# Kernel tuning notes

Hardware: AMD Instinct MI355X
Metric: run time of the kernel (lower is better)

## Reference

```python
import jax, jax.numpy as jnp
import numpy as np

G = 64          # offset groups == weight groups
KH = KW = 3
K = KH * KW
STRIDE = 2
PAD = 1


def _conv2d(x, w, b):
    out = jax.lax.conv_general_dilated(
        x, w, (STRIDE, STRIDE), [(PAD, PAD), (PAD, PAD)],
        dimension_numbers=("NCHW", "OIHW", "NCHW"))
    return out + b[None, :, None, None]


def _deform_core(x, offset, mask, w_deform):
    B, C, H, W = x.shape
    Ho, Wo = offset.shape[2], offset.shape[3]
    Cg = C // G
    # torchvision layout: channel = ((g*K + k)*2 + {0:dy,1:dx})
    off = offset.reshape(B, G, K, 2, Ho, Wo)
    dy, dx = off[:, :, :, 0], off[:, :, :, 1]          # [B,G,K,Ho,Wo]
    ki = (jnp.arange(K) // KW).astype(x.dtype)
    kj = (jnp.arange(K) % KW).astype(x.dtype)
    base_y = (jnp.arange(Ho, dtype=x.dtype) * STRIDE - PAD)[None, :, None] + ki[:, None, None]  # [K,Ho,1]
    base_x = (jnp.arange(Wo, dtype=x.dtype) * STRIDE - PAD)[None, None, :] + kj[:, None, None]  # [K,1,Wo]
    py = dy + base_y[None, None]                        # [B,G,K,Ho,Wo]
    px = dx + base_x[None, None]

    xg = x.reshape(B, G, Cg, H * W)
    y0 = jnp.floor(py)
    x0 = jnp.floor(px)
    wy = py - y0
    wx = px - x0
    KHW = K * Ho * Wo

    def gather(yc, xc, wgt):
        valid = (yc >= 0) & (yc <= H - 1) & (xc >= 0) & (xc <= W - 1)
        idx = (jnp.clip(yc, 0, H - 1) * W + jnp.clip(xc, 0, W - 1)).astype(jnp.int32)
        idx = jnp.broadcast_to(idx.reshape(B, G, 1, KHW), (B, G, Cg, KHW))
        v = jnp.take_along_axis(xg, idx, axis=3)
        return v * (wgt * valid.astype(x.dtype)).reshape(B, G, 1, KHW)

    val = (gather(y0, x0, (1 - wy) * (1 - wx))
           + gather(y0, x0 + 1, (1 - wy) * wx)
           + gather(y0 + 1, x0, wy * (1 - wx))
           + gather(y0 + 1, x0 + 1, wy * wx))
    cols = val.reshape(B, G, Cg, K, Ho, Wo) * mask.reshape(B, G, 1, K, Ho, Wo)
    # grouped conv as einsum: w_deform [C_out, Cg, 3, 3] -> [G, C_out//G, Cg, K]
    wg = w_deform.reshape(G, w_deform.shape[0] // G, Cg, K)
    out = jnp.einsum("bgckhw,gock->bgohw", cols, wg)
    return out.reshape(B, w_deform.shape[0], Ho, Wo)


def setup_inputs() -> dict:
    key = jax.random.key(0)
    ks = jax.random.split(key, 6)
    B, C, H, W = 2, 128, 256, 256
    x = jax.random.normal(ks[0], (B, C, H, W), dtype=jnp.float32)
    # small offset weights so sampled locations stay near the regular grid
    w_offset = jax.random.normal(ks[1], (G * 2 * K, C, 3, 3), dtype=jnp.float32) * 0.01
    b_offset = jax.random.normal(ks[2], (G * 2 * K,), dtype=jnp.float32) * 0.1
    w_mask = jax.random.normal(ks[3], (G * K, C, 3, 3), dtype=jnp.float32) * 0.01
    b_mask = jax.random.normal(ks[4], (G * K,), dtype=jnp.float32) * 0.1
    w_deform = jax.random.normal(ks[5], (C, C // G, 3, 3), dtype=jnp.float32) * (1.0 / np.sqrt((C // G) * K))
    return {"x": x, "w_offset": w_offset, "b_offset": b_offset,
            "w_mask": w_mask, "b_mask": b_mask, "w_deform": w_deform}


def reference(x, w_offset, b_offset, w_mask, b_mask, w_deform):
    offset = _conv2d(x, w_offset, b_offset)
    mask = jax.nn.sigmoid(_conv2d(x, w_mask, b_mask))
    return _deform_core(x, offset, mask, w_deform)
```

## Files before the change

kernel.cpp:

```cpp
#include <hip/hip_runtime.h>
#include <math.h>

#define B_SZ 2
#define H_IN 256
#define W_IN 256
#define HO 128
#define WO 128
#define CIN 128
#define CO_OFF 1152
#define CO_MSK 576
#define NG 64
#define KD 1152
#define KBY 2304
#define ND 32768
#define MPAD 1792
#define NT 18
#define XTROW_B 66048
#define XTIMG_B 17040384

typedef short short8 __attribute__((ext_vector_type(8)));
typedef float f32x4 __attribute__((ext_vector_type(4)));
typedef const unsigned int __attribute__((address_space(1))) gcu32;
typedef unsigned int __attribute__((address_space(3))) slu32;

__device__ __forceinline__ unsigned short f2b(float v) {
  union { float f; unsigned u; } a; a.f = v;
  unsigned r = a.u + 0x7FFF + ((a.u >> 16) & 1);
  return (unsigned short)(r >> 16);
}
__device__ __forceinline__ float b2f(unsigned short u) {
  union { unsigned u; float f; } a; a.u = ((unsigned)u) << 16;
  return a.f;
}

__global__ __launch_bounds__(256) void xpose(const float* __restrict__ x,
                                             unsigned short* __restrict__ xt) {
  const int bid = blockIdx.x;
  const int iyt = bid % 258;
  const int b = bid / 258;
  const int tid = threadIdx.x;
  char* rowp = (char*)xt + (size_t)b * XTIMG_B + (size_t)iyt * XTROW_B;
  const int iy = iyt - 1;
  const short8 z8 = {0, 0, 0, 0, 0, 0, 0, 0};

  if (iy < 0 || iy >= H_IN) {
    for (int i = tid; i < 4128; i += 256)
      *reinterpret_cast<short8*>(rowp + i * 16) = z8;
    return;
  }
  if (tid < 32) {
    int c = tid & 15;
    *reinterpret_cast<short8*>(rowp + ((tid >> 4) ? 257 * 256 : 0) + c * 16) = z8;
  }

  __shared__ float sX[32][68];
  const float* xb = x + (size_t)b * CIN * 65536 + iy * 256;
  for (int ci0 = 0; ci0 < CIN; ci0 += 32) {
    for (int ix0 = 0; ix0 < W_IN; ix0 += 64) {
      __syncthreads();
      {
        int ci_l = tid >> 3, f4 = tid & 7;
        const float4* src = reinterpret_cast<const float4*>(
            xb + (size_t)(ci0 + ci_l) * 65536 + ix0);
        *reinterpret_cast<float4*>(&sX[ci_l][f4 * 4]) = src[f4];
        *reinterpret_cast<float4*>(&sX[ci_l][(f4 + 8) * 4]) = src[f4 + 8];
      }
      __syncthreads();
      {
        int ix_l = tid >> 2, cq = (tid & 3) * 8;
        short8 o;
        #pragma unroll
        for (int e = 0; e < 8; e++) o[e] = (short)f2b(sX[cq + e][ix_l]);
        *reinterpret_cast<short8*>(rowp + (ix0 + ix_l + 1) * 256 + (ci0 + cq) * 2) = o;
      }
    }
  }
}

__global__ __launch_bounds__(256) void pack_w(const float* __restrict__ w_off,
                                              const float* __restrict__ w_msk,
                                              unsigned short* __restrict__ wb) {
  int i = blockIdx.x * 256 + threadIdx.x;
  int m = i / KD;
  int k = i - m * KD;
  int tap = k >> 7, ci = k & 127;
  int src = ci * 9 + tap;
  float v = 0.f;
  if (m < CO_OFF) v = w_off[(size_t)m * KD + src];
  else if (m < 1728) v = w_msk[(size_t)(m - CO_OFF) * KD + src];
  wb[i] = f2b(v);
}

__global__ __launch_bounds__(256, 2) void gemm_conv(
    const unsigned short* __restrict__ wb, const unsigned short* __restrict__ xt,
    const float* __restrict__ b_off, const float* __restrict__ b_msk,
    unsigned short* __restrict__ offs, unsigned short* __restrict__ mask)
{
  __shared__ __attribute__((aligned(128))) char lds[2][32768];

  const int bid = blockIdx.x;
  const int swz = (bid & 7) * 448 + (bid >> 3);
  const int m0 = (swz % 14) * 128;
  const int n0 = (swz / 14) * 128;
  const int ho = (n0 >> 7) & 127;
  const int b  = n0 >> 14;

  const int tid = threadIdx.x;
  const int l = tid & 63;
  const int w = tid >> 6;

  const int rl = l >> 3;
  const int kbsw = ((l & 7) << 4) ^ (rl << 4);

  const char* gA = (const char*)wb + (size_t)(m0 + (w & 1) * 64 + rl) * KBY + kbsw;
  const char* pB = (const char*)xt + (size_t)b * XTIMG_B
                 + ((w & 1) * 64 + rl) * 512 + kbsw;
  const int sb_off = (w & 1) * 8192;

  const int fr = l & 15;
  const int kq = (l >> 4) << 4;
  const int wm = (w >> 1) * 64;
  const int wn = (w & 1) * 64;

  f32x4 acc[4][4];
  #pragma unroll
  for (int a = 0; a < 4; a++)
    #pragma unroll
    for (int c = 0; c < 4; c++) acc[a][c] = (f32x4)(0.f);

  auto STAGE = [&](int kt, int bf) {
    if (w < 2) {
      const char* pa = gA + kt * 128;
      #pragma unroll
      for (int j = 0; j < 8; j++)
        __builtin_amdgcn_global_load_lds((gcu32*)(pa + (size_t)j * 8 * KBY),
                                         (slu32*)(&lds[bf][sb_off + j * 1024]), 16, 0, 0);
    } else {
      int tap = kt >> 1;
      int kh = (tap * 11) >> 5;
      int kw = tap - 3 * kh;
      const char* pb = pB + (2 * ho + kh) * XTROW_B + kw * 256 + (kt & 1) * 128;
      #pragma unroll
      for (int j = 0; j < 8; j++)
        __builtin_amdgcn_global_load_lds((gcu32*)(pb + j * 4096),
                                         (slu32*)(&lds[bf][16384 + sb_off + j * 1024]), 16, 0, 0);
    }
  };

  STAGE(0, 0);
  __syncthreads();

  int cur = 0;
  for (int t = 0; t < NT; t++) {
    if (t < NT - 1) STAGE(t + 1, cur ^ 1);

    const char* bufA = &lds[cur][0];
    const char* bufB = &lds[cur][16384];
    #pragma unroll
    for (int kk = 0; kk < 2; kk++) {
      short8 af[4], bf[4];
      #pragma unroll
      for (int mi = 0; mi < 4; mi++) {
        int row = wm + mi * 16 + fr;
        af[mi] = *(const short8*)(bufA + row * 128 + ((kk * 64 + kq) ^ ((row & 7) << 4)));
      }
      #pragma unroll
      for (int ni = 0; ni < 4; ni++) {
        int row = wn + ni * 16 + fr;
        bf[ni] = *(const short8*)(bufB + row * 128 + ((kk * 64 + kq) ^ ((row & 7) << 4)));
      }
      __builtin_amdgcn_s_setprio(1);
      #pragma unroll
      for (int mi = 0; mi < 4; mi++)
        #pragma unroll
        for (int ni = 0; ni < 4; ni++)
          asm("v_mfma_f32_16x16x32_bf16 %0, %1, %2, %0"
              : "+v"(acc[mi][ni]) : "v"(af[mi]), "v"(bf[ni]));
      __builtin_amdgcn_s_setprio(0);
    }
    __syncthreads();
    cur ^= 1;
  }

  const int nl0 = (n0 & 16383) + wn;
  const int rq = (l >> 4) * 4;
  #pragma unroll
  for (int mi = 0; mi < 4; mi++) {
    #pragma unroll
    for (int r = 0; r < 4; r++) {
      int m = m0 + wm + mi * 16 + rq + r;
      if (m < 1728) {
        bool ismk = (m >= CO_OFF);
        float bias = ismk ? b_msk[m - CO_OFF] : b_off[m];
        unsigned short* dst = ismk
            ? mask + (((size_t)(b * CO_MSK + (m - CO_OFF))) << 14)
            : offs + (((size_t)(b * CO_OFF + m)) << 14);
        #pragma unroll
        for (int ni = 0; ni < 4; ni++) {
          float v = acc[mi][ni][r] + bias;
          if (ismk) v = 1.f / (1.f + expf(-v));
          dst[nl0 + ni * 16 + fr] = f2b(v);
        }
      }
    }
  }
}

__global__ __launch_bounds__(256) void deform(
    const float* __restrict__ x, const unsigned short* __restrict__ offs,
    const unsigned short* __restrict__ mask, const float* __restrict__ wd,
    float* __restrict__ out)
{
  const int bid = blockIdx.x;
  const int hp = bid & 63;
  const int g  = (bid >> 6) & 63;
  const int b  = bid >> 12;
  const int tid = threadIdx.x;
  const int wo = tid & 127;
  const int ho = hp * 2 + (tid >> 7);

  __shared__ float swd[36];
  if (tid < 36) swd[tid] = wd[g * 36 + tid];
  __syncthreads();

  const float* xg = x + ((size_t)(b * CIN + g * 2)) * (H_IN * W_IN);
  float acc0 = 0.f, acc1 = 0.f;
  const int pbase = ((b * CO_OFF + g * 18) * HO + ho) * WO + wo;
  const int mbase = ((b * CO_MSK + g * 9) * HO + ho) * WO + wo;

  #pragma unroll
  for (int k = 0; k < 9; k++) {
    float dy = b2f(offs[pbase + (2 * k) * (HO * WO)]);
    float dx = b2f(offs[pbase + (2 * k + 1) * (HO * WO)]);
    float m  = b2f(mask[mbase + k * (HO * WO)]);
    float py = dy + (float)(ho * 2 - 1 + k / 3);
    float px = dx + (float)(wo * 2 - 1 + k % 3);
    float y0f = floorf(py), x0f = floorf(px);
    float wy = py - y0f, wx = px - x0f;
    float v0 = 0.f, v1 = 0.f;
    #pragma unroll
    for (int t = 0; t < 4; t++) {
      float yc = y0f + (float)(t >> 1);
      float xc = x0f + (float)(t & 1);
      float wgt = ((t >> 1) ? wy : 1.f - wy) * ((t & 1) ? wx : 1.f - wx);
      if (yc >= 0.f && yc <= (float)(H_IN - 1) && xc >= 0.f && xc <= (float)(W_IN - 1)) {
        int idx = (int)yc * W_IN + (int)xc;
        v0 += wgt * xg[idx];
        v1 += wgt * xg[H_IN * W_IN + idx];
      }
    }
    acc0 += m * (swd[0 * 18 + 0 * 9 + k] * v0 + swd[0 * 18 + 1 * 9 + k] * v1);
    acc1 += m * (swd[1 * 18 + 0 * 9 + k] * v0 + swd[1 * 18 + 1 * 9 + k] * v1);
  }

  out[((size_t)(b * CIN + g * 2 + 0) * HO + ho) * WO + wo] = acc0;
  out[((size_t)(b * CIN + g * 2 + 1) * HO + ho) * WO + wo] = acc1;
}

extern "C" void kernel_launch(void* const* d_in, const int* in_sizes, int n_in,
                              void* d_out, int out_size, void* d_ws, size_t ws_size,
                              hipStream_t stream) {
  const float* x     = (const float*)d_in[0];
  const float* w_off = (const float*)d_in[1];
  const float* b_off = (const float*)d_in[2];
  const float* w_msk = (const float*)d_in[3];
  const float* b_msk = (const float*)d_in[4];
  const float* w_def = (const float*)d_in[5];
  float* out = (float*)d_out;

  unsigned short* xt   = (unsigned short*)d_ws;
  unsigned short* wbf  = xt + (size_t)B_SZ * 258 * 258 * CIN;
  unsigned short* offs = wbf + (size_t)MPAD * KD;
  unsigned short* mask = offs + (size_t)B_SZ * CO_OFF * HO * WO;

  xpose<<<B_SZ * 258, 256, 0, stream>>>(x, xt);
  pack_w<<<(MPAD * KD) / 256, 256, 0, stream>>>(w_off, w_msk, wbf);
  gemm_conv<<<14 * 256, 256, 0, stream>>>(wbf, xt, b_off, b_msk, offs, mask);
  deform<<<B_SZ * NG * (HO / 2), 256, 0, stream>>>(x, offs, mask, w_def, out);
}
```

Measured before the change: 396.3 us.

## Enlarge conv GEMM tile to 256x256 with 8 waves and interleaved LDS pipeline

```diff
diff --git a/kernel.cpp b/kernel.cpp
--- a/kernel.cpp
+++ b/kernel.cpp
@@ -14,7 +14,7 @@
 #define KBY 2304
 #define ND 32768
 #define MPAD 1792
-#define NT 18
+#define NTK 18
 #define XTROW_B 66048
 #define XTIMG_B 17040384
 
@@ -91,19 +91,19 @@
   wb[i] = f2b(v);
 }
 
-__global__ __launch_bounds__(256, 2) void gemm_conv(
+__global__ __launch_bounds__(512) void gemm_conv(
     const unsigned short* __restrict__ wb, const unsigned short* __restrict__ xt,
     const float* __restrict__ b_off, const float* __restrict__ b_msk,
     unsigned short* __restrict__ offs, unsigned short* __restrict__ mask)
 {
-  __shared__ __attribute__((aligned(128))) char lds[2][32768];
+  __shared__ __attribute__((aligned(128))) char lds[2][65536];
 
   const int bid = blockIdx.x;
-  const int swz = (bid & 7) * 448 + (bid >> 3);
-  const int m0 = (swz % 14) * 128;
-  const int n0 = (swz / 14) * 128;
-  const int ho = (n0 >> 7) & 127;
+  const int swz = (bid & 7) * 112 + (bid >> 3);
+  const int m0 = (swz % 7) * 256;
+  const int n0 = (swz / 7) * 256;
   const int b  = n0 >> 14;
+  const int ho_base = (n0 & 16383) >> 7;
 
   const int tid = threadIdx.x;
   const int l = tid & 63;
@@ -112,80 +112,89 @@
   const int rl = l >> 3;
   const int kbsw = ((l & 7) << 4) ^ (rl << 4);
 
-  const char* gA = (const char*)wb + (size_t)(m0 + (w & 1) * 64 + rl) * KBY + kbsw;
+  const char* pA = (const char*)wb + (size_t)(m0 + 32 * w + rl) * KBY + kbsw;
   const char* pB = (const char*)xt + (size_t)b * XTIMG_B
-                 + ((w & 1) * 64 + rl) * 512 + kbsw;
-  const int sb_off = (w & 1) * 8192;
+                 + (size_t)(2 * (ho_base + (w >> 2))) * XTROW_B
+                 + (2 * ((w & 3) * 32 + rl)) * 256 + kbsw;
 
   const int fr = l & 15;
   const int kq = (l >> 4) << 4;
-  const int wm = (w >> 1) * 64;
-  const int wn = (w & 1) * 64;
-
-  f32x4 acc[4][4];
+  const int wm = (w >> 2) * 128;
+  const int wn = (w & 3) * 64;
+
+  f32x4 acc[8][4];
   #pragma unroll
-  for (int a = 0; a < 4; a++)
+  for (int a = 0; a < 8; a++)
     #pragma unroll
     for (int c = 0; c < 4; c++) acc[a][c] = (f32x4)(0.f);
 
-  auto STAGE = [&](int kt, int bf) {
-    if (w < 2) {
-      const char* pa = gA + kt * 128;
-      #pragma unroll
-      for (int j = 0; j < 8; j++)
-        __builtin_amdgcn_global_load_lds((gcu32*)(pa + (size_t)j * 8 * KBY),
-                                         (slu32*)(&lds[bf][sb_off + j * 1024]), 16, 0, 0);
-    } else {
-      int tap = kt >> 1;
-      int kh = (tap * 11) >> 5;
-      int kw = tap - 3 * kh;
-      const char* pb = pB + (2 * ho + kh) * XTROW_B + kw * 256 + (kt & 1) * 128;
-      #pragma unroll
-      for (int j = 0; j < 8; j++)
-        __builtin_amdgcn_global_load_lds((gcu32*)(pb + j * 4096),
-                                         (slu32*)(&lds[bf][16384 + sb_off + j * 1024]), 16, 0, 0);
-    }
-  };
-
-  STAGE(0, 0);
-  __syncthreads();
-
-  int cur = 0;
-  for (int t = 0; t < NT; t++) {
-    if (t < NT - 1) STAGE(t + 1, cur ^ 1);
-
-    const char* bufA = &lds[cur][0];
-    const char* bufB = &lds[cur][16384];
-    #pragma unroll
-    for (int kk = 0; kk < 2; kk++) {
-      short8 af[4], bf[4];
-      #pragma unroll
-      for (int mi = 0; mi < 4; mi++) {
-        int row = wm + mi * 16 + fr;
-        af[mi] = *(const short8*)(bufA + row * 128 + ((kk * 64 + kq) ^ ((row & 7) << 4)));
-      }
-      #pragma unroll
-      for (int ni = 0; ni < 4; ni++) {
-        int row = wn + ni * 16 + fr;
-        bf[ni] = *(const short8*)(bufB + row * 128 + ((kk * 64 + kq) ^ ((row & 7) << 4)));
-      }
-      __builtin_amdgcn_s_setprio(1);
-      #pragma unroll
-      for (int mi = 0; mi < 4; mi++)
-        #pragma unroll
-        for (int ni = 0; ni < 4; ni++)
-          asm("v_mfma_f32_16x16x32_bf16 %0, %1, %2, %0"
-              : "+v"(acc[mi][ni]) : "v"(af[mi]), "v"(bf[ni]));
-      __builtin_amdgcn_s_setprio(0);
-    }
-    __syncthreads();
-    cur ^= 1;
+  short8 af[4][2];
+  short8 bfr[4][2];
+
+#define STAGE_A(kt, bf) { const char* s_ = pA + (kt) * 128; \
+  char* d_ = &lds[bf][0] + w * 4096; \
+  _Pragma("unroll") for (int j_ = 0; j_ < 4; j_++) \
+    __builtin_amdgcn_global_load_lds((gcu32*)(s_ + (size_t)j_ * 8 * KBY), \
+                                     (slu32*)(d_ + j_ * 1024), 16, 0, 0); }
+
+#define STAGE_B(kt, bf) { int tap_ = (kt) >> 1; int kh_ = tap_ / 3; int kw_ = tap_ - 3 * kh_; \
+  const char* s_ = pB + kh_ * XTROW_B + kw_ * 256 + ((kt) & 1) * 128; \
+  char* d_ = &lds[bf][32768] + w * 4096; \
+  _Pragma("unroll") for (int j_ = 0; j_ < 4; j_++) \
+    __builtin_amdgcn_global_load_lds((gcu32*)(s_ + j_ * 4096), \
+                                     (slu32*)(d_ + j_ * 1024), 16, 0, 0); }
+
+#define LDA(mih, bf) _Pragma("unroll") for (int mi_ = 0; mi_ < 4; mi_++) \
+  _Pragma("unroll") for (int kk_ = 0; kk_ < 2; kk_++) { \
+    int row_ = wm + ((mih) * 4 + mi_) * 16 + fr; \
+    af[mi_][kk_] = *(const short8*)(&lds[bf][0] + row_ * 128 + ((kk_ * 64 + kq) ^ ((row_ & 7) << 4))); }
+
+#define LDB(nih, bf) _Pragma("unroll") for (int ni_ = 0; ni_ < 2; ni_++) \
+  _Pragma("unroll") for (int kk_ = 0; kk_ < 2; kk_++) { \
+    int row_ = wn + ((nih) * 2 + ni_) * 16 + fr; \
+    bfr[(nih) * 2 + ni_][kk_] = *(const short8*)(&lds[bf][32768] + row_ * 128 + ((kk_ * 64 + kq) ^ ((row_ & 7) << 4))); }
+
+#define MMQ(mih, nih) __builtin_amdgcn_s_setprio(1); \
+  _Pragma("unroll") for (int mi_ = 0; mi_ < 4; mi_++) \
+    _Pragma("unroll") for (int ni_ = 0; ni_ < 2; ni_++) \
+      _Pragma("unroll") for (int kk_ = 0; kk_ < 2; kk_++) \
+        asm("v_mfma_f32_16x16x32_bf16 %0, %1, %2, %0" \
+            : "+v"(acc[(mih) * 4 + mi_][(nih) * 2 + ni_]) \
+            : "v"(af[mi_][kk_]), "v"(bfr[(nih) * 2 + ni_][kk_])); \
+  __builtin_amdgcn_s_setprio(0);
+
+#define BAR __builtin_amdgcn_s_barrier();
+#define WAITVM(n) asm volatile("s_waitcnt vmcnt(" #n ")" ::: "memory");
+
+  STAGE_B(0, 0) STAGE_A(0, 0) STAGE_B(1, 1) STAGE_A(1, 1)
+  WAITVM(8) BAR
+
+  for (int i = 0; i < 9; i++) {
+    const bool st = (i < 8);
+    LDA(0, 0) LDB(0, 0)
+    BAR MMQ(0, 0) BAR
+    LDB(1, 0)
+    BAR MMQ(0, 1) BAR
+    LDA(1, 0)
+    if (st) { STAGE_B(2 * i + 2, 0) }
+    BAR MMQ(1, 0) BAR
+    if (st) { STAGE_A(2 * i + 2, 0) WAITVM(8) } else { WAITVM(0) }
+    BAR MMQ(1, 1) BAR
+    LDA(0, 1) LDB(0, 1)
+    BAR MMQ(0, 0) BAR
+    LDB(1, 1)
+    BAR MMQ(0, 1) BAR
+    LDA(1, 1)
+    if (st) { STAGE_B(2 * i + 3, 1) }
+    BAR MMQ(1, 0) BAR
+    if (st) { STAGE_A(2 * i + 3, 1) WAITVM(8) } else { WAITVM(0) }
+    BAR MMQ(1, 1) BAR
   }
 
   const int nl0 = (n0 & 16383) + wn;
   const int rq = (l >> 4) * 4;
   #pragma unroll
-  for (int mi = 0; mi < 4; mi++) {
+  for (int mi = 0; mi < 8; mi++) {
     #pragma unroll
     for (int r = 0; r < 4; r++) {
       int m = m0 + wm + mi * 16 + rq + r;
@@ -275,6 +284,6 @@
 
   xpose<<<B_SZ * 258, 256, 0, stream>>>(x, xt);
   pack_w<<<(MPAD * KD) / 256, 256, 0, stream>>>(w_off, w_msk, wbf);
-  gemm_conv<<<14 * 256, 256, 0, stream>>>(wbf, xt, b_off, b_msk, offs, mask);
+  gemm_conv<<<896, 512, 0, stream>>>(wbf, xt, b_off, b_msk, offs, mask);
   deform<<<B_SZ * NG * (HO / 2), 256, 0, stream>>>(x, offs, mask, w_def, out);
 }
```

Result: slower. 405.5 us (+2.3%).

## Sample deform inputs from padded bf16 NHWC buffer and single-buffer GEMM LDS

Applied to the files above, without the earlier changes.

```diff
diff --git a/kernel.cpp b/kernel.cpp
--- a/kernel.cpp
+++ b/kernel.cpp
@@ -14,7 +14,7 @@
 #define KBY 2304
 #define ND 32768
 #define MPAD 1792
-#define NT 18
+#define NTK 18
 #define XTROW_B 66048
 #define XTIMG_B 17040384
 
@@ -96,7 +96,8 @@
     const float* __restrict__ b_off, const float* __restrict__ b_msk,
     unsigned short* __restrict__ offs, unsigned short* __restrict__ mask)
 {
-  __shared__ __attribute__((aligned(128))) char lds[2][32768];
+  __shared__ __attribute__((aligned(128))) char sA[16384];
+  __shared__ __attribute__((aligned(128))) char sB[16384];
 
   const int bid = blockIdx.x;
   const int swz = (bid & 7) * 448 + (bid >> 3);
@@ -111,11 +112,11 @@
 
   const int rl = l >> 3;
   const int kbsw = ((l & 7) << 4) ^ (rl << 4);
-
   const char* gA = (const char*)wb + (size_t)(m0 + (w & 1) * 64 + rl) * KBY + kbsw;
   const char* pB = (const char*)xt + (size_t)b * XTIMG_B
-                 + ((w & 1) * 64 + rl) * 512 + kbsw;
-  const int sb_off = (w & 1) * 8192;
+                 + (size_t)(2 * ho) * XTROW_B
+                 + (2 * ((w & 1) * 64 + rl)) * 256 + kbsw;
+  char* sbase = ((w < 2) ? sA : sB) + (w & 1) * 8192;
 
   const int fr = l & 15;
   const int kq = (l >> 4) << 4;
@@ -128,58 +129,45 @@
     #pragma unroll
     for (int c = 0; c < 4; c++) acc[a][c] = (f32x4)(0.f);
 
-  auto STAGE = [&](int kt, int bf) {
+  for (int kt = 0; kt < NTK; kt++) {
+    __syncthreads();
     if (w < 2) {
       const char* pa = gA + kt * 128;
       #pragma unroll
       for (int j = 0; j < 8; j++)
         __builtin_amdgcn_global_load_lds((gcu32*)(pa + (size_t)j * 8 * KBY),
-                                         (slu32*)(&lds[bf][sb_off + j * 1024]), 16, 0, 0);
+                                         (slu32*)(sbase + j * 1024), 16, 0, 0);
     } else {
       int tap = kt >> 1;
-      int kh = (tap * 11) >> 5;
-      int kw = tap - 3 * kh;
-      const char* pb = pB + (2 * ho + kh) * XTROW_B + kw * 256 + (kt & 1) * 128;
+      int kh = tap / 3, kw = tap - 3 * kh;
+      const char* pb = pB + kh * XTROW_B + kw * 256 + (kt & 1) * 128;
       #pragma unroll
       for (int j = 0; j < 8; j++)
         __builtin_amdgcn_global_load_lds((gcu32*)(pb + j * 4096),
-                                         (slu32*)(&lds[bf][16384 + sb_off + j * 1024]), 16, 0, 0);
-    }
-  };
-
-  STAGE(0, 0);
-  __syncthreads();
-
-  int cur = 0;
-  for (int t = 0; t < NT; t++) {
-    if (t < NT - 1) STAGE(t + 1, cur ^ 1);
-
-    const char* bufA = &lds[cur][0];
-    const char* bufB = &lds[cur][16384];
+                                         (slu32*)(sbase + j * 1024), 16, 0, 0);
+    }
+    __syncthreads();
+
     #pragma unroll
     for (int kk = 0; kk < 2; kk++) {
       short8 af[4], bf[4];
       #pragma unroll
       for (int mi = 0; mi < 4; mi++) {
         int row = wm + mi * 16 + fr;
-        af[mi] = *(const short8*)(bufA + row * 128 + ((kk * 64 + kq) ^ ((row & 7) << 4)));
+        af[mi] = *(const short8*)(sA + row * 128 + ((kk * 64 + kq) ^ ((row & 7) << 4)));
       }
       #pragma unroll
       for (int ni = 0; ni < 4; ni++) {
         int row = wn + ni * 16 + fr;
-        bf[ni] = *(const short8*)(bufB + row * 128 + ((kk * 64 + kq) ^ ((row & 7) << 4)));
-      }
-      __builtin_amdgcn_s_setprio(1);
+        bf[ni] = *(const short8*)(sB + row * 128 + ((kk * 64 + kq) ^ ((row & 7) << 4)));
+      }
       #pragma unroll
       for (int mi = 0; mi < 4; mi++)
         #pragma unroll
         for (int ni = 0; ni < 4; ni++)
           asm("v_mfma_f32_16x16x32_bf16 %0, %1, %2, %0"
               : "+v"(acc[mi][ni]) : "v"(af[mi]), "v"(bf[ni]));
-      __builtin_amdgcn_s_setprio(0);
-    }
-    __syncthreads();
-    cur ^= 1;
+    }
   }
 
   const int nl0 = (n0 & 16383) + wn;
@@ -207,7 +195,7 @@
 }
 
 __global__ __launch_bounds__(256) void deform(
-    const float* __restrict__ x, const unsigned short* __restrict__ offs,
+    const unsigned short* __restrict__ xt, const unsigned short* __restrict__ offs,
     const unsigned short* __restrict__ mask, const float* __restrict__ wd,
     float* __restrict__ out)
 {
@@ -223,34 +211,40 @@
   if (tid < 36) swd[tid] = wd[g * 36 + tid];
   __syncthreads();
 
-  const float* xg = x + ((size_t)(b * CIN + g * 2)) * (H_IN * W_IN);
+  const char* bb = (const char*)xt + (size_t)b * XTIMG_B + 4 * g;
   float acc0 = 0.f, acc1 = 0.f;
   const int pbase = ((b * CO_OFF + g * 18) * HO + ho) * WO + wo;
   const int mbase = ((b * CO_MSK + g * 9) * HO + ho) * WO + wo;
 
   #pragma unroll
   for (int k = 0; k < 9; k++) {
-    float dy = b2f(offs[pbase + (2 * k) * (HO * WO)]);
-    float dx = b2f(offs[pbase + (2 * k + 1) * (HO * WO)]);
-    float m  = b2f(mask[mbase + k * (HO * WO)]);
+    float dy = b2f(offs[pbase + (2 * k) * 16384]);
+    float dx = b2f(offs[pbase + (2 * k + 1) * 16384]);
+    float m  = b2f(mask[mbase + k * 16384]);
     float py = dy + (float)(ho * 2 - 1 + k / 3);
     float px = dx + (float)(wo * 2 - 1 + k % 3);
     float y0f = floorf(py), x0f = floorf(px);
     float wy = py - y0f, wx = px - x0f;
-    float v0 = 0.f, v1 = 0.f;
-    #pragma unroll
-    for (int t = 0; t < 4; t++) {
-      float yc = y0f + (float)(t >> 1);
-      float xc = x0f + (float)(t & 1);
-      float wgt = ((t >> 1) ? wy : 1.f - wy) * ((t & 1) ? wx : 1.f - wx);
-      if (yc >= 0.f && yc <= (float)(H_IN - 1) && xc >= 0.f && xc <= (float)(W_IN - 1)) {
-        int idx = (int)yc * W_IN + (int)xc;
-        v0 += wgt * xg[idx];
-        v1 += wgt * xg[H_IN * W_IN + idx];
-      }
-    }
-    acc0 += m * (swd[0 * 18 + 0 * 9 + k] * v0 + swd[0 * 18 + 1 * 9 + k] * v1);
-    acc1 += m * (swd[1 * 18 + 0 * 9 + k] * v0 + swd[1 * 18 + 1 * 9 + k] * v1);
+    int iy0 = (int)fminf(fmaxf(y0f,       -1.f), 256.f) + 1;
+    int iy1 = (int)fminf(fmaxf(y0f + 1.f, -1.f), 256.f) + 1;
+    int ix0 = (int)fminf(fmaxf(x0f,       -1.f), 256.f) + 1;
+    int ix1 = (int)fminf(fmaxf(x0f + 1.f, -1.f), 256.f) + 1;
+    const char* r0 = bb + (size_t)iy0 * XTROW_B;
+    const char* r1 = bb + (size_t)iy1 * XTROW_B;
+    unsigned u00 = *(const unsigned*)(r0 + ix0 * 256);
+    unsigned u01 = *(const unsigned*)(r0 + ix1 * 256);
+    unsigned u10 = *(const unsigned*)(r1 + ix0 * 256);
+    unsigned u11 = *(const unsigned*)(r1 + ix1 * 256);
+    float w11 = wy * wx;
+    float w10 = wy - w11;
+    float w01 = wx - w11;
+    float w00 = 1.f - wy - w01;
+    float v0 = w00 * b2f((unsigned short)u00) + w01 * b2f((unsigned short)u01)
+             + w10 * b2f((unsigned short)u10) + w11 * b2f((unsigned short)u11);
+    float v1 = w00 * b2f((unsigned short)(u00 >> 16)) + w01 * b2f((unsigned short)(u01 >> 16))
+             + w10 * b2f((unsigned short)(u10 >> 16)) + w11 * b2f((unsigned short)(u11 >> 16));
+    acc0 += m * (swd[k] * v0 + swd[9 + k] * v1);
+    acc1 += m * (swd[18 + k] * v0 + swd[27 + k] * v1);
   }
 
   out[((size_t)(b * CIN + g * 2 + 0) * HO + ho) * WO + wo] = acc0;
@@ -276,5 +270,5 @@
   xpose<<<B_SZ * 258, 256, 0, stream>>>(x, xt);
   pack_w<<<(MPAD * KD) / 256, 256, 0, stream>>>(w_off, w_msk, wbf);
   gemm_conv<<<14 * 256, 256, 0, stream>>>(wbf, xt, b_off, b_msk, offs, mask);
-  deform<<<B_SZ * NG * (HO / 2), 256, 0, stream>>>(x, offs, mask, w_def, out);
-}
+  deform<<<B_SZ * NG * (HO / 2), 256, 0, stream>>>(xt, offs, mask, w_def, out);
+}
```

Result: slower. 547.6 us (+38.2%).
